# Optimization experiments

Measured on AMD Instinct MI355X. Metric: run time of the kernel, lower is better.

The kernel has to match this reference:

```python
import jax, jax.numpy as jnp
import numpy as np

N, D = 8192, 1024
TEMPERATURE = 0.1
EPS = 1e-8

def setup_inputs() -> dict:
    key = jax.random.key(0)
    k1, k2 = jax.random.split(key)
    emb = jax.random.normal(k1, (N, D), dtype=jnp.float32)
    # docstring: embeddings are normalized
    emb = emb / jnp.linalg.norm(emb, axis=1, keepdims=True)
    labels = jax.random.randint(k2, (N,), 0, 2, dtype=jnp.int32)
    return {"embeddings": emb, "labels": labels}

def reference(embeddings, labels):
    lab = labels.astype(embeddings.dtype)            # (N,)
    sim = jnp.matmul(embeddings, embeddings.T) / TEMPERATURE  # (N, N)
    exp_sim = jnp.exp(sim)                           # original uses raw exp (no max-subtract)
    diag = jnp.diagonal(exp_sim)                     # self-similarity exp(1/T)
    # all_sim excludes self; pos_sim = other reference rows (labels==1, j != i)
    all_sum = exp_sim.sum(axis=1) - diag             # (N,)
    pos_sum = exp_sim @ lab - diag * lab             # subtract self only when i is ref
    loss_per_row = -jnp.log(pos_sum / (all_sum + EPS))
    n_ref = lab.sum()
    loss = jnp.sum(jnp.where(lab > 0, loss_per_row, 0.0)) / jnp.maximum(n_ref, 1.0)
    # original returns 0.0 when fewer than 2 reference rows
    return jnp.where(n_ref < 2, jnp.array(0.0, embeddings.dtype), loss)
```

## Files before the change

### kernel.cpp

```cpp
#include <hip/hip_runtime.h>
#include <hip/hip_bf16.h>
#include <cstdint>
#include <cstddef>

#define NROWS 8192
#define DIM   1024
#define BMR 128
#define BNC 128
#define BK  64
#define NBLK 2080
#define EPS 1e-8f
#define PRESCALE 3.798288f

typedef short  bf16x8  __attribute__((ext_vector_type(8)));
typedef float  floatx4 __attribute__((ext_vector_type(4)));

typedef __attribute__((address_space(1))) const void CGV;
typedef __attribute__((address_space(3))) void LV;

__device__ __forceinline__ void async_load16(const void* g, void* l) {
    __builtin_amdgcn_global_load_lds((CGV*)g, (LV*)l, 16, 0, 0);
}

__device__ __forceinline__ unsigned short f2bf_rne(float f) {
    union { float f; unsigned u; } c; c.f = f;
    unsigned u = c.u;
    unsigned r = (u + 0x7fffu + ((u >> 16) & 1u)) >> 16;
    return (unsigned short)r;
}

__global__ __launch_bounds__(256) void convert_kernel(
    const float* __restrict__ in, unsigned short* __restrict__ out,
    float* __restrict__ accum )
{
    int i = (blockIdx.x * 256 + threadIdx.x) * 4;
    float4 v = *(const float4*)(in + i);
    ushort4 o;
    o.x = f2bf_rne(v.x * PRESCALE);
    o.y = f2bf_rne(v.y * PRESCALE);
    o.z = f2bf_rne(v.z * PRESCALE);
    o.w = f2bf_rne(v.w * PRESCALE);
    *(ushort4*)(out + i) = o;
    if (blockIdx.x < (2 * NROWS) / 256)
        accum[blockIdx.x * 256 + threadIdx.x] = 0.0f;
}

__global__ __launch_bounds__(128, 2) void gemm_fused_kernel(
    const unsigned short* __restrict__ E,
    const int*            __restrict__ labels,
    float*                __restrict__ all_sum,
    float*                __restrict__ pos_sum)
{
    __shared__ __align__(16) unsigned short sA[BMR * BK];
    __shared__ __align__(16) unsigned short sB[BNC * BK];

    const int tid  = threadIdx.x;
    const int lane = tid & 63;
    const int w    = tid >> 6;
    const int colw = lane & 15;
    const int quad = lane >> 4;

    const int b = blockIdx.x;
    const int t = (b & 7) * 260 + (b >> 3);
    int bi = (int)((sqrtf(8.0f * (float)t + 1.0f) - 1.0f) * 0.5f);
    while ((bi + 1) * (bi + 2) / 2 <= t) ++bi;
    while (bi * (bi + 1) / 2 > t) --bi;
    const int bj = t - bi * (bi + 1) / 2;

    const int rBase = bi * BMR;
    const int cBase = bj * BNC;

    const int srow = tid >> 3;
    const int scol = (((tid & 7) ^ (srow & 7)) << 3);
    const int e0   = tid * 8;

    floatx4 acc[4][8];
    #pragma unroll
    for (int i = 0; i < 4; ++i)
        #pragma unroll
        for (int j = 0; j < 8; ++j)
            acc[i][j] = (floatx4)0.0f;

    const int swz   = colw & 7;
    const int aRow0 = (w * 64 + colw) * BK;
    const int bRow0 = colw * BK;

    const size_t gA0 = (size_t)(rBase + srow) * DIM + scol;
    const size_t gB0 = (size_t)(cBase + srow) * DIM + scol;
    const size_t rstep = (size_t)16 * DIM;

    for (int k0 = 0; k0 < DIM; k0 += BK) {
        __syncthreads();
        #pragma unroll
        for (int j = 0; j < 8; ++j)
            async_load16(E + gA0 + j * rstep + k0, &sA[e0 + j * 1024]);
        #pragma unroll
        for (int j = 0; j < 8; ++j)
            async_load16(E + gB0 + j * rstep + k0, &sB[e0 + j * 1024]);
        __syncthreads();

        #pragma unroll
        for (int h = 0; h < 2; ++h) {
            const int cOff = (((h << 2) | quad) ^ swz) << 3;
            bf16x8 aF[4], bF[8];
            #pragma unroll
            for (int mt = 0; mt < 4; ++mt)
                aF[mt] = *(const bf16x8*)&sA[aRow0 + mt * 16 * BK + cOff];
            #pragma unroll
            for (int nt = 0; nt < 8; ++nt)
                bF[nt] = *(const bf16x8*)&sB[bRow0 + nt * 16 * BK + cOff];

            #pragma unroll
            for (int mt = 0; mt < 4; ++mt)
                #pragma unroll
                for (int nt = 0; nt < 8; ++nt)
                    acc[mt][nt] = __builtin_amdgcn_mfma_f32_16x16x32_bf16(
                        aF[mt], bF[nt], acc[mt][nt], 0, 0, 0);
        }
    }

    float labc[8];
    int   gcol[8];
    #pragma unroll
    for (int nt = 0; nt < 8; ++nt) {
        gcol[nt] = cBase + nt * 16 + colw;
        labc[nt] = (float)labels[gcol[nt]];
    }

    float colAll[8] = {0.f, 0.f, 0.f, 0.f, 0.f, 0.f, 0.f, 0.f};
    float colPos[8] = {0.f, 0.f, 0.f, 0.f, 0.f, 0.f, 0.f, 0.f};

    #pragma unroll
    for (int mt = 0; mt < 4; ++mt) {
        const int growBase = rBase + w * 64 + mt * 16 + quad * 4;
        #pragma unroll
        for (int r = 0; r < 4; ++r) {
            const int grow = growBase + r;
            const float labr = (float)labels[grow];
            float sAll = 0.f, sPos = 0.f;
            #pragma unroll
            for (int nt = 0; nt < 8; ++nt) {
                float ev = exp2f(acc[mt][nt][r]);
                ev = (grow > gcol[nt]) ? ev : 0.0f;
                sAll += ev;
                sPos += ev * labc[nt];
                colAll[nt] += ev;
                colPos[nt] += ev * labr;
            }
            #pragma unroll
            for (int off = 1; off < 16; off <<= 1) {
                sAll += __shfl_xor(sAll, off);
                sPos += __shfl_xor(sPos, off);
            }
            if (colw == 0 && sAll != 0.f) {
                atomicAdd(&all_sum[grow], sAll);
                atomicAdd(&pos_sum[grow], sPos);
            }
        }
    }

    #pragma unroll
    for (int nt = 0; nt < 8; ++nt) {
        float a = colAll[nt], p = colPos[nt];
        a += __shfl_xor(a, 16);  p += __shfl_xor(p, 16);
        a += __shfl_xor(a, 32);  p += __shfl_xor(p, 32);
        if (quad == 0 && a != 0.f) {
            atomicAdd(&all_sum[gcol[nt]], a);
            atomicAdd(&pos_sum[gcol[nt]], p);
        }
    }
}

__global__ __launch_bounds__(1024) void finalize_kernel(
    const float* __restrict__ all_sum,
    const float* __restrict__ pos_sum,
    const int*   __restrict__ labels,
    float*       __restrict__ out)
{
    __shared__ float sSum[1024];
    __shared__ float sCnt[1024];
    const int tid = threadIdx.x;
    float lsum = 0.f, lcnt = 0.f;
    for (int i = tid; i < NROWS; i += 1024) {
        if (labels[i] > 0) {
            float p = pos_sum[i];
            float a = all_sum[i] + EPS;
            lsum += -logf(p / a);
            lcnt += 1.0f;
        }
    }
    sSum[tid] = lsum;
    sCnt[tid] = lcnt;
    __syncthreads();
    for (int s = 512; s > 0; s >>= 1) {
        if (tid < s) { sSum[tid] += sSum[tid + s]; sCnt[tid] += sCnt[tid + s]; }
        __syncthreads();
    }
    if (tid == 0) {
        float n = sCnt[0];
        out[0] = (n < 2.0f) ? 0.0f : sSum[0] / fmaxf(n, 1.0f);
    }
}

extern "C" void kernel_launch(void* const* d_in, const int* in_sizes, int n_in,
                              void* d_out, int out_size, void* d_ws, size_t ws_size,
                              hipStream_t stream) {
    const float* emb    = (const float*)d_in[0];
    const int*   labels = (const int*)d_in[1];
    float*       out    = (float*)d_out;

    unsigned short* Ebf = (unsigned short*)d_ws;
    const size_t embBytes = (size_t)NROWS * DIM * sizeof(unsigned short);
    float* all_sum = (float*)((char*)d_ws + embBytes);
    float* pos_sum = all_sum + NROWS;

    convert_kernel<<<(NROWS * DIM) / (4 * 256), 256, 0, stream>>>(emb, Ebf, all_sum);

    gemm_fused_kernel<<<NBLK, 128, 0, stream>>>(Ebf, labels, all_sum, pos_sum);

    finalize_kernel<<<1, 1024, 0, stream>>>(all_sum, pos_sum, labels, out);
}
```

Before: 183.7 us.

## Load A fragments directly from global into registers with double-buffered prefetch

The A tile no longer goes through LDS. Each wave loads its own A MFMA fragments straight from global memory into registers, double-buffered so that the next K-step's fragments are prefetched while the current step runs. This halves LDS traffic and LDS footprint, which may allow higher occupancy. In exchange it raises register pressure (16 bf16x8 A registers plus 128 accumulator floats), fully unrolls the K loop, and issues uncoalesced 16-byte global loads per lane that depend on L2 hits.

```diff
diff --git a/kernel.cpp b/kernel.cpp
--- a/kernel.cpp
+++ b/kernel.cpp
@@ -8,6 +8,7 @@
 #define BMR 128
 #define BNC 128
 #define BK  64
+#define NITER (DIM / BK)
 #define NBLK 2080
 #define EPS 1e-8f
 #define PRESCALE 3.798288f
@@ -51,7 +52,6 @@
     float*                __restrict__ all_sum,
     float*                __restrict__ pos_sum)
 {
-    __shared__ __align__(16) unsigned short sA[BMR * BK];
     __shared__ __align__(16) unsigned short sB[BNC * BK];
 
     const int tid  = threadIdx.x;
@@ -82,40 +82,53 @@
             acc[i][j] = (floatx4)0.0f;
 
     const int swz   = colw & 7;
-    const int aRow0 = (w * 64 + colw) * BK;
     const int bRow0 = colw * BK;
 
-    const size_t gA0 = (size_t)(rBase + srow) * DIM + scol;
+    const unsigned short* aB[4];
+    #pragma unroll
+    for (int mt = 0; mt < 4; ++mt)
+        aB[mt] = E + (size_t)(rBase + w * 64 + mt * 16 + colw) * DIM + quad * 8;
+
     const size_t gB0 = (size_t)(cBase + srow) * DIM + scol;
     const size_t rstep = (size_t)16 * DIM;
 
-    for (int k0 = 0; k0 < DIM; k0 += BK) {
+    bf16x8 aR[2][8];
+    #pragma unroll
+    for (int mt = 0; mt < 4; ++mt)
+        #pragma unroll
+        for (int h = 0; h < 2; ++h)
+            aR[0][mt * 2 + h] = *(const bf16x8*)(aB[mt] + h * 32);
+
+    #pragma unroll
+    for (int it = 0; it < NITER; ++it) {
+        const int cur = it & 1;
+        const int k0  = it * BK;
         __syncthreads();
-        #pragma unroll
-        for (int j = 0; j < 8; ++j)
-            async_load16(E + gA0 + j * rstep + k0, &sA[e0 + j * 1024]);
         #pragma unroll
         for (int j = 0; j < 8; ++j)
             async_load16(E + gB0 + j * rstep + k0, &sB[e0 + j * 1024]);
         __syncthreads();
 
+        if (it + 1 < NITER) {
+            #pragma unroll
+            for (int mt = 0; mt < 4; ++mt)
+                #pragma unroll
+                for (int h = 0; h < 2; ++h)
+                    aR[1 - cur][mt * 2 + h] =
+                        *(const bf16x8*)(aB[mt] + k0 + BK + h * 32);
+        }
+
         #pragma unroll
         for (int h = 0; h < 2; ++h) {
             const int cOff = (((h << 2) | quad) ^ swz) << 3;
-            bf16x8 aF[4], bF[8];
-            #pragma unroll
-            for (int mt = 0; mt < 4; ++mt)
-                aF[mt] = *(const bf16x8*)&sA[aRow0 + mt * 16 * BK + cOff];
-            #pragma unroll
-            for (int nt = 0; nt < 8; ++nt)
-                bF[nt] = *(const bf16x8*)&sB[bRow0 + nt * 16 * BK + cOff];
-
-            #pragma unroll
-            for (int mt = 0; mt < 4; ++mt)
+            #pragma unroll
+            for (int nt = 0; nt < 8; ++nt) {
+                bf16x8 bF = *(const bf16x8*)&sB[bRow0 + nt * 16 * BK + cOff];
                 #pragma unroll
-                for (int nt = 0; nt < 8; ++nt)
+                for (int mt = 0; mt < 4; ++mt)
                     acc[mt][nt] = __builtin_amdgcn_mfma_f32_16x16x32_bf16(
-                        aF[mt], bF[nt], acc[mt][nt], 0, 0, 0);
+                        aR[cur][mt * 2 + h], bF, acc[mt][nt], 0, 0, 0);
+            }
         }
     }
 
```

Result: slower. 199.3 us (+8.5%).
